# Kernel optimization log

Measured on AMD Instinct MI355X. Metric: run time of the kernel, lower is better.

Reference implementation:

```python
import jax, jax.numpy as jnp
import numpy as np

N_ATOMS = 100000
N_BONDS = 400000
ATOM_FDIM = 133
BOND_FDIM = 147
HIDDEN = 300
DEPTH = 3


def setup_inputs() -> dict:
    key = jax.random.key(0)
    ks = jax.random.split(key, 10)
    f_atoms = jax.random.normal(ks[0], (N_ATOMS, ATOM_FDIM), dtype=jnp.float32)
    f_bonds = jax.random.normal(ks[1], (N_BONDS, BOND_FDIM), dtype=jnp.float32)
    b2a = jax.random.randint(ks[2], (N_BONDS,), 0, N_ATOMS)
    b2revb = jax.random.randint(ks[3], (N_BONDS,), 0, N_BONDS)
    s_i = 1.0 / np.sqrt(BOND_FDIM)
    s_h = 1.0 / np.sqrt(HIDDEN)
    s_o = 1.0 / np.sqrt(ATOM_FDIM + HIDDEN)
    Wi_w = jax.random.uniform(ks[4], (HIDDEN, BOND_FDIM), jnp.float32, -s_i, s_i)
    Wi_b = jax.random.uniform(ks[5], (HIDDEN,), jnp.float32, -s_i, s_i)
    Wh_w = jax.random.uniform(ks[6], (HIDDEN, HIDDEN), jnp.float32, -s_h, s_h)
    Wh_b = jax.random.uniform(ks[7], (HIDDEN,), jnp.float32, -s_h, s_h)
    Wo_w = jax.random.uniform(ks[8], (HIDDEN, ATOM_FDIM + HIDDEN), jnp.float32, -s_o, s_o)
    Wo_b = jax.random.uniform(ks[9], (HIDDEN,), jnp.float32, -s_o, s_o)
    return {"f_atoms": f_atoms, "f_bonds": f_bonds, "b2a": b2a, "b2revb": b2revb,
            "Wi_w": Wi_w, "Wi_b": Wi_b, "Wh_w": Wh_w, "Wh_b": Wh_b,
            "Wo_w": Wo_w, "Wo_b": Wo_b}


def reference(f_atoms, f_bonds, b2a, b2revb, Wi_w, Wi_b, Wh_w, Wh_b, Wo_w, Wo_b):
    n_atoms = f_atoms.shape[0]
    # initial bond messages: [n_bonds, hidden]
    H_bonds = jax.nn.relu(f_bonds @ Wi_w.T + Wi_b)
    dest = b2a[b2revb]  # destination atom of each directed bond
    for _ in range(DEPTH - 1):
        # scatter-add bond messages onto destination atoms
        sum_msgs = jax.ops.segment_sum(H_bonds, dest, num_segments=n_atoms)
        # gather back to bonds from source atoms, subtract reverse-bond message
        msgs = sum_msgs[b2a] - H_bonds[b2revb]
        H_bonds = jax.nn.relu(H_bonds + msgs @ Wh_w.T + Wh_b)
    sum_msgs = jax.ops.segment_sum(H_bonds, dest, num_segments=n_atoms)
    H_atoms = jax.nn.relu(jnp.concatenate([f_atoms, sum_msgs], axis=1) @ Wo_w.T + Wo_b)
    return (H_atoms, H_bonds)
```

## Files before the change

kernel.cpp:

```cpp
#include <hip/hip_runtime.h>
#include <hip/hip_bf16.h>

#define NB 400000
#define NA 100000
#define AFD 133
#define BFD 147
#define HID 300
#define NP  320
#define SMP 304
#define NT  98

typedef short short8 __attribute__((ext_vector_type(8)));
typedef float f32x4 __attribute__((ext_vector_type(4)));

__device__ __forceinline__ ushort f2b(float f) {
    union { float f; unsigned u; } v; v.f = f;
    unsigned r = v.u + 0x7fffu + ((v.u >> 16) & 1u);
    return (ushort)(r >> 16);
}
__device__ __forceinline__ float b2f(ushort u) {
    union { unsigned u; float f; } v; v.u = ((unsigned)u) << 16;
    return v.f;
}

#define GLDS(gp, lp) __builtin_amdgcn_global_load_lds( \
    (const __attribute__((address_space(1))) void*)(gp), \
    (__attribute__((address_space(3))) void*)(lp), 16, 0, 0)


__global__ void pad_w_k(const float* __restrict__ W, ushort* __restrict__ Wp,
                        int N, int K, int Kp) {
    int idx = blockIdx.x * 256 + threadIdx.x;
    if (idx >= NP * Kp) return;
    int n = idx / Kp, k = idx - n * Kp;
    int t = k >> 5, kk = k & 31;
    int g = kk >> 3, s = kk & 7;
    int gp = g ^ ((n >> 1) & 3);
    ushort v = (n < N && k < K) ? f2b(W[n * K + k]) : (ushort)0;
    Wp[(size_t)t * 10240 + n * 32 + gp * 8 + s] = v;
}

__global__ void pad_bias_k(const float* __restrict__ bh, float* __restrict__ bhp) {
    int i = blockIdx.x * 256 + threadIdx.x;
    if (i < NP) bhp[i] = (i < HID) ? bh[i] : 0.f;
}

__global__ void dest_k(const int* __restrict__ b2a, const int* __restrict__ b2revb,
                       int* __restrict__ dest) {
    int b = blockIdx.x * 256 + threadIdx.x;
    if (b < NB) dest[b] = b2a[b2revb[b]];
}

__global__ void count_k(const int* __restrict__ dest, int* __restrict__ cnt) {
    int b = blockIdx.x * 256 + threadIdx.x;
    if (b < NB) atomicAdd(&cnt[dest[b]], 1);
}

__global__ void scanA_k(const int* __restrict__ cnt, int* __restrict__ tsum) {
    __shared__ int sm[256];
    const int tid = threadIdx.x;
    int base = blockIdx.x * 1024 + tid * 4;
    int s = 0;
#pragma unroll
    for (int j = 0; j < 4; ++j) { int i = base + j; if (i < NA) s += cnt[i]; }
    sm[tid] = s; __syncthreads();
    for (int o = 128; o > 0; o >>= 1) {
        if (tid < o) sm[tid] += sm[tid + o];
        __syncthreads();
    }
    if (tid == 0) tsum[blockIdx.x] = sm[0];
}

__global__ void scanB_k(const int* __restrict__ tsum, int* __restrict__ toff,
                        int* __restrict__ rs) {
    if (threadIdx.x == 0) {
        int run = 0;
        for (int t = 0; t < NT; ++t) { toff[t] = run; run += tsum[t]; }
        rs[NA] = run;
    }
}

__global__ void scanC_k(const int* __restrict__ cnt, const int* __restrict__ toff,
                        int* __restrict__ rs) {
    __shared__ int sm[256];
    const int tid = threadIdx.x;
    int base = blockIdx.x * 1024 + tid * 4;
    int v[4]; int s = 0;
#pragma unroll
    for (int j = 0; j < 4; ++j) {
        v[j] = (base + j < NA) ? cnt[base + j] : 0;
        s += v[j];
    }
    sm[tid] = s; __syncthreads();
    for (int o = 1; o < 256; o <<= 1) {
        int x = (tid >= o) ? sm[tid - o] : 0;
        __syncthreads();
        sm[tid] += x;
        __syncthreads();
    }
    int acc = sm[tid] - s + toff[blockIdx.x];
#pragma unroll
    for (int j = 0; j < 4; ++j) {
        if (base + j < NA) rs[base + j] = acc;
        acc += v[j];
    }
}

__global__ void scatter_k(const int* __restrict__ dest, const int* __restrict__ rs,
                          int* __restrict__ cur, int* __restrict__ bl) {
    int b = blockIdx.x * 256 + threadIdx.x;
    if (b >= NB) return;
    int a = dest[b];
    int pos = rs[a] + atomicAdd(&cur[a], 1);
    bl[pos] = b;
}

template<int MODE>
__global__ __launch_bounds__(512) void gemm_k(
    const float* __restrict__ F1, const float* __restrict__ Sum,
    const ushort* __restrict__ W, const float* __restrict__ bias,
    ushort* __restrict__ Cb, float* __restrict__ Cf, int M)
{
    constexpr int KP = (MODE == 0) ? 192 : 448;
    constexpr int TILES = KP / 32;
    static_assert(KP % 64 == 0 && TILES % 2 == 0, "XOR swizzle needs 128B rows, even tiles");
    __shared__ ushort As[128 * KP];
    __shared__ ushort Bs[2][320 * 32];

    const int tid = threadIdx.x;
    const int w = tid >> 6, lane = tid & 63;
    const int wr = w >> 2, wc = w & 3;
    const int g = lane >> 4, lr = lane & 15;
    const int m0 = blockIdx.x * 128;

    {
        const int row = tid >> 2, q = tid & 3;
        int grow = m0 + row;
        if (MODE == 2 && grow >= M) grow = M - 1;
        const int axw = (row & 7) << 4;
        char* abase = (char*)As + (size_t)row * (KP * 2);
#pragma unroll
        for (int t = 0; t < TILES; ++t) {
            const int k0 = t * 32 + q * 8;
            ushort o[8];
            if (MODE == 0) {
                const float* src = F1 + (size_t)grow * BFD;
#pragma unroll
                for (int s = 0; s < 8; ++s)
                    o[s] = (k0 + s < BFD) ? f2b(src[k0 + s]) : (ushort)0;
            } else {
#pragma unroll
                for (int s = 0; s < 8; ++s) {
                    int k = k0 + s;
                    float x = 0.f;
                    if (k < AFD) x = F1[(size_t)grow * AFD + k];
                    else if (k < AFD + SMP) x = Sum[(size_t)grow * SMP + (k - AFD)];
                    o[s] = f2b(x);
                }
            }
            ushort* dst = (ushort*)(abase + ((t * 64 + q * 16) ^ axw));
            *(ushort4*)dst       = make_ushort4(o[0], o[1], o[2], o[3]);
            *(ushort4*)(dst + 4) = make_ushort4(o[4], o[5], o[6], o[7]);
        }
    }

    auto stageB = [&](int t, int buf) {
        const ushort* wt = W + (size_t)t * 10240;
        ushort* bs = &Bs[buf][0];
        GLDS(wt + (size_t)w * 512 + lane * 8,        bs + w * 512);
        GLDS(wt + (size_t)(w + 8) * 512 + lane * 8,  bs + (w + 8) * 512);
        if (w < 4)
            GLDS(wt + (size_t)(w + 16) * 512 + lane * 8, bs + (w + 16) * 512);
    };

    f32x4 acc[4][5];
#pragma unroll
    for (int mi = 0; mi < 4; ++mi)
#pragma unroll
        for (int ni = 0; ni < 5; ++ni) acc[mi][ni] = (f32x4){0.f, 0.f, 0.f, 0.f};

    stageB(0, 0);
    __syncthreads();

    const int raxw = (lr & 7) << 4;
    const int bswz = (lr >> 1) & 3;
    for (int t = 0; t < TILES; ++t) {
        if (t + 1 < TILES) stageB(t + 1, (t + 1) & 1);
        const ushort* bs = &Bs[t & 1][0];
        short8 af[4];
#pragma unroll
        for (int mi = 0; mi < 4; ++mi) {
            const int r = wr * 64 + mi * 16 + lr;
            af[mi] = *(const short8*)((const char*)As + (size_t)r * (KP * 2)
                                      + ((t * 64 + g * 16) ^ raxw));
        }
#pragma unroll
        for (int ni = 0; ni < 5; ++ni) {
            const int c = wc * 80 + ni * 16 + lr;
            short8 bf = *(const short8*)&bs[c * 32 + ((g ^ bswz) << 3)];
#pragma unroll
            for (int mi = 0; mi < 4; ++mi)
                acc[mi][ni] = __builtin_amdgcn_mfma_f32_16x16x32_bf16(af[mi], bf, acc[mi][ni], 0, 0, 0);
        }
        __syncthreads();
    }

#pragma unroll
    for (int ni = 0; ni < 5; ++ni) {
        const int col = wc * 80 + ni * 16 + lr;
        const float bv = (col < HID) ? bias[col] : 0.f;
#pragma unroll
        for (int mi = 0; mi < 4; ++mi) {
            const int row0 = m0 + wr * 64 + mi * 16 + g * 4;
#pragma unroll
            for (int r = 0; r < 4; ++r) {
                const int row = row0 + r;
                float v = fmaxf(acc[mi][ni][r] + bv, 0.f);
                if (MODE == 2) {
                    if (col < HID && row < M) Cf[(size_t)row * HID + col] = v;
                } else {
                    Cb[(size_t)row * NP + col] = f2b(v);
                }
            }
        }
    }
}

__global__ __launch_bounds__(512) void gemm_a_k(
    const ushort* __restrict__ A, const ushort* __restrict__ W,
    ushort* __restrict__ C, int M)
{
    __shared__ ushort As[2][4][128][8];
    __shared__ ushort Bs[2][320 * 32];
    const int tid = threadIdx.x;
    const int w = tid >> 6, lane = tid & 63;
    const int wr = w >> 2, wc = w & 3;
    const int g = lane >> 4, lr = lane & 15;
    const int m0 = blockIdx.x * 128;

    const int q = w >> 1, r0 = (w & 1) * 64;
    int srow = m0 + r0 + lane; if (srow >= M) srow = M - 1;
    const ushort* aglob = A + (size_t)srow * NP + q * 8;

    f32x4 acc[4][5];
#pragma unroll
    for (int mi = 0; mi < 4; ++mi)
#pragma unroll
        for (int ni = 0; ni < 5; ++ni) acc[mi][ni] = (f32x4){0.f, 0.f, 0.f, 0.f};

    auto stageA = [&](int t, int buf) { GLDS(aglob + t * 32, &As[buf][q][r0][0]); };
    auto stageB = [&](int t, int buf) {
        const ushort* wt = W + (size_t)t * 10240;
        ushort* bs = &Bs[buf][0];
        GLDS(wt + (size_t)w * 512 + lane * 8,        bs + w * 512);
        GLDS(wt + (size_t)(w + 8) * 512 + lane * 8,  bs + (w + 8) * 512);
        if (w < 4)
            GLDS(wt + (size_t)(w + 16) * 512 + lane * 8, bs + (w + 16) * 512);
    };

    stageA(0, 0); stageB(0, 0);
    __syncthreads();

    const int bswz = (lr >> 1) & 3;
    for (int t = 0; t < 10; ++t) {
        if (t < 9) { stageA(t + 1, (t + 1) & 1); stageB(t + 1, (t + 1) & 1); }
        const int buf = t & 1;
        short8 af[4];
#pragma unroll
        for (int mi = 0; mi < 4; ++mi)
            af[mi] = *(const short8*)&As[buf][g][wr * 64 + mi * 16 + lr][0];
#pragma unroll
        for (int ni = 0; ni < 5; ++ni) {
            const int c = wc * 80 + ni * 16 + lr;
            short8 bf = *(const short8*)&Bs[buf][c * 32 + ((g ^ bswz) << 3)];
#pragma unroll
            for (int mi = 0; mi < 4; ++mi)
                acc[mi][ni] = __builtin_amdgcn_mfma_f32_16x16x32_bf16(af[mi], bf, acc[mi][ni], 0, 0, 0);
        }
        __syncthreads();
    }

#pragma unroll
    for (int ni = 0; ni < 5; ++ni) {
        const int col = wc * 80 + ni * 16 + lr;
#pragma unroll
        for (int mi = 0; mi < 4; ++mi) {
            const int row0 = m0 + wr * 64 + mi * 16 + g * 4;
#pragma unroll
            for (int r = 0; r < 4; ++r)
                if (row0 + r < M) C[(size_t)(row0 + r) * NP + col] = f2b(acc[mi][ni][r]);
        }
    }
}

template<bool OUTF>
__global__ __launch_bounds__(512) void gemm_u_k(
    const ushort* __restrict__ HbIn, const ushort* __restrict__ W,
    const ushort* __restrict__ SYa,
    const int* __restrict__ b2a, const int* __restrict__ b2revb,
    const float* __restrict__ bhp,
    ushort* __restrict__ HbOut, float* __restrict__ Hbonds)
{
    __shared__ ushort As[2][4][128][8];
    __shared__ ushort Bs[2][320 * 32];
    const int tid = threadIdx.x;
    const int w = tid >> 6, lane = tid & 63;
    const int wr = w >> 2, wc = w & 3;
    const int g = lane >> 4, lr = lane & 15;
    const int m0 = blockIdx.x * 128;

    const int q = w >> 1, r0 = (w & 1) * 64;
    const int rrow = b2revb[m0 + r0 + lane];
    const ushort* aglob = HbIn + (size_t)rrow * NP + q * 8;

    f32x4 acc[4][5];
#pragma unroll
    for (int mi = 0; mi < 4; ++mi)
#pragma unroll
        for (int ni = 0; ni < 5; ++ni) acc[mi][ni] = (f32x4){0.f, 0.f, 0.f, 0.f};

    auto stageA = [&](int t, int buf) { GLDS(aglob + t * 32, &As[buf][q][r0][0]); };
    auto stageB = [&](int t, int buf) {
        const ushort* wt = W + (size_t)t * 10240;
        ushort* bs = &Bs[buf][0];
        GLDS(wt + (size_t)w * 512 + lane * 8,        bs + w * 512);
        GLDS(wt + (size_t)(w + 8) * 512 + lane * 8,  bs + (w + 8) * 512);
        if (w < 4)
            GLDS(wt + (size_t)(w + 16) * 512 + lane * 8, bs + (w + 16) * 512);
    };

    stageA(0, 0); stageB(0, 0);
    __syncthreads();

    const int bswz = (lr >> 1) & 3;
    for (int t = 0; t < 10; ++t) {
        if (t < 9) { stageA(t + 1, (t + 1) & 1); stageB(t + 1, (t + 1) & 1); }
        const int buf = t & 1;
        short8 af[4];
#pragma unroll
        for (int mi = 0; mi < 4; ++mi)
            af[mi] = *(const short8*)&As[buf][g][wr * 64 + mi * 16 + lr][0];
#pragma unroll
        for (int ni = 0; ni < 5; ++ni) {
            const int c = wc * 80 + ni * 16 + lr;
            short8 bf = *(const short8*)&Bs[buf][c * 32 + ((g ^ bswz) << 3)];
#pragma unroll
            for (int mi = 0; mi < 4; ++mi)
                acc[mi][ni] = __builtin_amdgcn_mfma_f32_16x16x32_bf16(af[mi], bf, acc[mi][ni], 0, 0, 0);
        }
        __syncthreads();
    }

    float bv[5];
#pragma unroll
    for (int ni = 0; ni < 5; ++ni) bv[ni] = bhp[wc * 80 + ni * 16 + lr];
#pragma unroll
    for (int mi = 0; mi < 4; ++mi) {
#pragma unroll
        for (int r = 0; r < 4; ++r) {
            const int row = m0 + wr * 64 + mi * 16 + g * 4 + r;
            const int sa = b2a[row];
            const ushort* hp = &HbIn[(size_t)row * NP];
            const ushort* sp = &SYa[(size_t)sa * NP];
#pragma unroll
            for (int ni = 0; ni < 5; ++ni) {
                const int col = wc * 80 + ni * 16 + lr;
                float v = fmaxf(b2f(hp[col]) + b2f(sp[col]) - acc[mi][ni][r] + bv[ni], 0.f);
                HbOut[(size_t)row * NP + col] = f2b(v);
                if (OUTF && col < HID) Hbonds[(size_t)row * HID + col] = v;
            }
        }
    }
}

__global__ void seg_sum_bf16_k(const ushort* __restrict__ H, const int* __restrict__ rs,
                               const int* __restrict__ bl, ushort* __restrict__ SH) {
    int idx = blockIdx.x * 256 + threadIdx.x;
    if (idx >= NA * 40) return;
    int a = idx / 40, c = (idx - a * 40) * 8;
    int s0 = rs[a], s1 = rs[a + 1];
    float acc[8] = {0.f, 0.f, 0.f, 0.f, 0.f, 0.f, 0.f, 0.f};
    for (int j = s0; j < s1; ++j) {
        const ushort* p = &H[(size_t)bl[j] * NP + c];
        ushort4 u0 = *(const ushort4*)p, u1 = *(const ushort4*)(p + 4);
        acc[0] += b2f(u0.x); acc[1] += b2f(u0.y);
        acc[2] += b2f(u0.z); acc[3] += b2f(u0.w);
        acc[4] += b2f(u1.x); acc[5] += b2f(u1.y);
        acc[6] += b2f(u1.z); acc[7] += b2f(u1.w);
    }
    ushort* dst = &SH[(size_t)a * NP + c];
    *(ushort4*)dst       = make_ushort4(f2b(acc[0]), f2b(acc[1]), f2b(acc[2]), f2b(acc[3]));
    *(ushort4*)(dst + 4) = make_ushort4(f2b(acc[4]), f2b(acc[5]), f2b(acc[6]), f2b(acc[7]));
}

__global__ void seg_sum_csr_k(const ushort* __restrict__ Hb, const int* __restrict__ rs,
                              const int* __restrict__ bl, float* __restrict__ sum) {
    int idx = blockIdx.x * 256 + threadIdx.x;
    if (idx >= NA * 38) return;
    int a = idx / 38, c = (idx - a * 38) * 8;
    int s0 = rs[a], s1 = rs[a + 1];
    float acc[8] = {0.f, 0.f, 0.f, 0.f, 0.f, 0.f, 0.f, 0.f};
    for (int j = s0; j < s1; ++j) {
        const ushort* p = &Hb[(size_t)bl[j] * NP + c];
        ushort4 u0 = *(const ushort4*)p, u1 = *(const ushort4*)(p + 4);
        acc[0] += b2f(u0.x); acc[1] += b2f(u0.y);
        acc[2] += b2f(u0.z); acc[3] += b2f(u0.w);
        acc[4] += b2f(u1.x); acc[5] += b2f(u1.y);
        acc[6] += b2f(u1.z); acc[7] += b2f(u1.w);
    }
    float* dst = &sum[(size_t)a * SMP + c];
    *(float4*)dst       = make_float4(acc[0], acc[1], acc[2], acc[3]);
    *(float4*)(dst + 4) = make_float4(acc[4], acc[5], acc[6], acc[7]);
}

extern "C" void kernel_launch(void* const* d_in, const int* in_sizes, int n_in,
                              void* d_out, int out_size, void* d_ws, size_t ws_size,
                              hipStream_t stream) {
    const float* f_atoms = (const float*)d_in[0];
    const float* f_bonds = (const float*)d_in[1];
    const int*   b2a     = (const int*)d_in[2];
    const int*   b2revb  = (const int*)d_in[3];
    const float* Wi_w    = (const float*)d_in[4];
    const float* Wi_b    = (const float*)d_in[5];
    const float* Wh_w    = (const float*)d_in[6];
    const float* Wh_b    = (const float*)d_in[7];
    const float* Wo_w    = (const float*)d_in[8];
    const float* Wo_b    = (const float*)d_in[9];
    float* out = (float*)d_out;

    char* ws = (char*)d_ws;
    ushort* Hb0  = (ushort*)ws;            ws += (size_t)NB * NP * 2;
    ushort* Hb1  = (ushort*)ws;            ws += (size_t)NB * NP * 2;
    ushort* SHb  = (ushort*)ws;            ws += (size_t)NA * NP * 2;
    ushort* SYa  = (ushort*)ws;            ws += (size_t)NA * NP * 2;
    float*  sum  = (float*)ws;             ws += (size_t)NA * SMP * 4;
    int*    dest = (int*)ws;               ws += (size_t)NB * 4;
    ushort* Wp0  = (ushort*)ws;            ws += (size_t)6  * 10240 * 2;
    ushort* Wp1  = (ushort*)ws;            ws += (size_t)10 * 10240 * 2;
    ushort* Wp2  = (ushort*)ws;            ws += (size_t)14 * 10240 * 2;
    float*  bhp  = (float*)ws;             ws += (size_t)NP * 4;
    int*    cnt  = (int*)ws;               ws += (size_t)NA * 4;
    int*    cur  = (int*)ws;               ws += (size_t)NA * 4;
    int*    rs   = (int*)ws;               ws += (size_t)(NA + 1) * 4;
    int*    bl   = (int*)ws;               ws += (size_t)NB * 4;
    int*    tsum = (int*)ws;               ws += 128 * 4;
    int*    toff = (int*)ws;               ws += 128 * 4;
    float* Hatoms = out;
    float* Hbonds = out + (size_t)NA * HID;

    pad_w_k<<<(NP * 192 + 255) / 256, 256, 0, stream>>>(Wi_w, Wp0, HID, BFD, 192);
    pad_w_k<<<(NP * NP  + 255) / 256, 256, 0, stream>>>(Wh_w, Wp1, HID, HID, NP);
    pad_w_k<<<(NP * 448 + 255) / 256, 256, 0, stream>>>(Wo_w, Wp2, HID, AFD + HID, 448);
    pad_bias_k<<<2, 256, 0, stream>>>(Wh_b, bhp);
    dest_k<<<(NB + 255) / 256, 256, 0, stream>>>(b2a, b2revb, dest);
    hipMemsetAsync(cnt, 0, (size_t)NA * 4, stream);
    hipMemsetAsync(cur, 0, (size_t)NA * 4, stream);
    count_k<<<(NB + 255) / 256, 256, 0, stream>>>(dest, cnt);
    scanA_k<<<NT, 256, 0, stream>>>(cnt, tsum);
    scanB_k<<<1, 64, 0, stream>>>(tsum, toff, rs);
    scanC_k<<<NT, 256, 0, stream>>>(cnt, toff, rs);
    scatter_k<<<(NB + 255) / 256, 256, 0, stream>>>(dest, rs, cur, bl);

    gemm_k<0><<<NB / 128, 512, 0, stream>>>(
        f_bonds, nullptr, Wp0, Wi_b, Hb0, nullptr, NB);

    seg_sum_bf16_k<<<(NA * 40 + 255) / 256, 256, 0, stream>>>(Hb0, rs, bl, SHb);
    gemm_a_k<<<(NA + 127) / 128, 512, 0, stream>>>(SHb, Wp1, SYa, NA);
    gemm_u_k<false><<<NB / 128, 512, 0, stream>>>(
        Hb0, Wp1, SYa, b2a, b2revb, bhp, Hb1, nullptr);

    seg_sum_bf16_k<<<(NA * 40 + 255) / 256, 256, 0, stream>>>(Hb1, rs, bl, SHb);
    gemm_a_k<<<(NA + 127) / 128, 512, 0, stream>>>(SHb, Wp1, SYa, NA);
    gemm_u_k<true><<<NB / 128, 512, 0, stream>>>(
        Hb1, Wp1, SYa, b2a, b2revb, bhp, Hb0, Hbonds);

    seg_sum_csr_k<<<(NA * 38 + 255) / 256, 256, 0, stream>>>(Hb0, rs, bl, sum);
    gemm_k<2><<<(NA + 127) / 128, 512, 0, stream>>>(
        f_atoms, sum, Wp2, Wo_b, nullptr, Hatoms, NA);
}
```

Baseline: 1.680 ms.

## Stage GEMM epilogues through LDS for coalesced stores; reuse bf16 segment sum

The epilogues of the initial bond GEMM and the update GEMM now write accumulators into shared memory one column quarter at a time. Threads then read them back row-contiguous, so the global loads and stores for HbIn, SYa, HbOut and Hbonds are vectorized and coalesced instead of scattered 2-byte writes. The final segment sum reuses the bf16 kernel writing into SHb, and the output GEMM reads bf16 directly, removing the fp32 sum buffer and its conversion. The cost is four extra barrier phases per block plus an LDS round trip, and a slight precision loss because the final atom sums are now rounded to bf16.

```diff
diff --git a/kernel.cpp b/kernel.cpp
--- a/kernel.cpp
+++ b/kernel.cpp
@@ -7,7 +7,6 @@
 #define BFD 147
 #define HID 300
 #define NP  320
-#define SMP 304
 #define NT  98
 
 typedef short short8 __attribute__((ext_vector_type(8)));
@@ -117,15 +116,15 @@
 
 template<int MODE>
 __global__ __launch_bounds__(512) void gemm_k(
-    const float* __restrict__ F1, const float* __restrict__ Sum,
+    const float* __restrict__ F1, const ushort* __restrict__ SHb,
     const ushort* __restrict__ W, const float* __restrict__ bias,
     ushort* __restrict__ Cb, float* __restrict__ Cf, int M)
 {
     constexpr int KP = (MODE == 0) ? 192 : 448;
     constexpr int TILES = KP / 32;
     static_assert(KP % 64 == 0 && TILES % 2 == 0, "XOR swizzle needs 128B rows, even tiles");
-    __shared__ ushort As[128 * KP];
-    __shared__ ushort Bs[2][320 * 32];
+    __shared__ char smem[(128 * KP + 2 * 10240) * 2];
+    ushort (*Bs)[10240] = (ushort (*)[10240])(smem + 128 * KP * 2);
 
     const int tid = threadIdx.x;
     const int w = tid >> 6, lane = tid & 63;
@@ -138,7 +137,7 @@
         int grow = m0 + row;
         if (MODE == 2 && grow >= M) grow = M - 1;
         const int axw = (row & 7) << 4;
-        char* abase = (char*)As + (size_t)row * (KP * 2);
+        char* abase = smem + (size_t)row * (KP * 2);
 #pragma unroll
         for (int t = 0; t < TILES; ++t) {
             const int k0 = t * 32 + q * 8;
@@ -152,10 +151,8 @@
 #pragma unroll
                 for (int s = 0; s < 8; ++s) {
                     int k = k0 + s;
-                    float x = 0.f;
-                    if (k < AFD) x = F1[(size_t)grow * AFD + k];
-                    else if (k < AFD + SMP) x = Sum[(size_t)grow * SMP + (k - AFD)];
-                    o[s] = f2b(x);
+                    o[s] = (k < AFD) ? f2b(F1[(size_t)grow * AFD + k])
+                                     : SHb[(size_t)grow * NP + (k - AFD)];
                 }
             }
             ushort* dst = (ushort*)(abase + ((t * 64 + q * 16) ^ axw));
@@ -191,7 +188,7 @@
 #pragma unroll
         for (int mi = 0; mi < 4; ++mi) {
             const int r = wr * 64 + mi * 16 + lr;
-            af[mi] = *(const short8*)((const char*)As + (size_t)r * (KP * 2)
+            af[mi] = *(const short8*)(smem + (size_t)r * (KP * 2)
                                       + ((t * 64 + g * 16) ^ raxw));
         }
 #pragma unroll
@@ -205,21 +202,47 @@
         __syncthreads();
     }
 
-#pragma unroll
-    for (int ni = 0; ni < 5; ++ni) {
-        const int col = wc * 80 + ni * 16 + lr;
-        const float bv = (col < HID) ? bias[col] : 0.f;
-#pragma unroll
-        for (int mi = 0; mi < 4; ++mi) {
-            const int row0 = m0 + wr * 64 + mi * 16 + g * 4;
-#pragma unroll
-            for (int r = 0; r < 4; ++r) {
-                const int row = row0 + r;
-                float v = fmaxf(acc[mi][ni][r] + bv, 0.f);
-                if (MODE == 2) {
+    if (MODE == 0) {
+        float* EP = (float*)smem;
+        for (int ph = 0; ph < 4; ++ph) {
+            __syncthreads();
+            if (wc == ph) {
+#pragma unroll
+                for (int mi = 0; mi < 4; ++mi)
+#pragma unroll
+                    for (int ni = 0; ni < 5; ++ni) {
+                        const int ec = ni * 16 + lr;
+#pragma unroll
+                        for (int r = 0; r < 4; ++r)
+                            EP[(wr * 64 + mi * 16 + g * 4 + r) * 84 + ec] = acc[mi][ni][r];
+                    }
+            }
+            __syncthreads();
+            for (int it2 = tid; it2 < 2560; it2 += 512) {
+                const int row = it2 / 20, cc = (it2 - row * 20) * 4;
+                const int grow = m0 + row;
+                const int col = ph * 80 + cc;
+                float4 a = *(const float4*)&EP[row * 84 + cc];
+                float4 bb = (col < HID) ? *(const float4*)&bias[col]
+                                        : make_float4(0.f, 0.f, 0.f, 0.f);
+                *(ushort4*)&Cb[(size_t)grow * NP + col] =
+                    make_ushort4(f2b(fmaxf(a.x + bb.x, 0.f)), f2b(fmaxf(a.y + bb.y, 0.f)),
+                                 f2b(fmaxf(a.z + bb.z, 0.f)), f2b(fmaxf(a.w + bb.w, 0.f)));
+            }
+        }
+    } else {
+#pragma unroll
+        for (int ni = 0; ni < 5; ++ni) {
+            const int col = wc * 80 + ni * 16 + lr;
+            const float bv = (col < HID) ? bias[col] : 0.f;
+#pragma unroll
+            for (int mi = 0; mi < 4; ++mi) {
+                const int row0 = m0 + wr * 64 + mi * 16 + g * 4;
+#pragma unroll
+                for (int r = 0; r < 4; ++r) {
+                    const int row = row0 + r;
+                    float v = fmaxf(acc[mi][ni][r] + bv, 0.f);
                     if (col < HID && row < M) Cf[(size_t)row * HID + col] = v;
-                } else {
-                    Cb[(size_t)row * NP + col] = f2b(v);
                 }
             }
         }
@@ -231,7 +254,7 @@
     ushort* __restrict__ C, int M)
 {
     __shared__ ushort As[2][4][128][8];
-    __shared__ ushort Bs[2][320 * 32];
+    __shared__ ushort Bs[2][10240];
     const int tid = threadIdx.x;
     const int w = tid >> 6, lane = tid & 63;
     const int wr = w >> 2, wc = w & 3;
@@ -301,8 +324,9 @@
     const float* __restrict__ bhp,
     ushort* __restrict__ HbOut, float* __restrict__ Hbonds)
 {
-    __shared__ ushort As[2][4][128][8];
-    __shared__ ushort Bs[2][320 * 32];
+    __shared__ char smem[57344];
+    ushort (*As)[4][128][8] = (ushort (*)[4][128][8])smem;
+    ushort (*Bs)[10240] = (ushort (*)[10240])(smem + 16384);
     const int tid = threadIdx.x;
     const int w = tid >> 6, lane = tid & 63;
     const int wr = w >> 2, wc = w & 3;
@@ -351,24 +375,38 @@
         __syncthreads();
     }
 
-    float bv[5];
-#pragma unroll
-    for (int ni = 0; ni < 5; ++ni) bv[ni] = bhp[wc * 80 + ni * 16 + lr];
-#pragma unroll
-    for (int mi = 0; mi < 4; ++mi) {
-#pragma unroll
-        for (int r = 0; r < 4; ++r) {
-            const int row = m0 + wr * 64 + mi * 16 + g * 4 + r;
-            const int sa = b2a[row];
-            const ushort* hp = &HbIn[(size_t)row * NP];
-            const ushort* sp = &SYa[(size_t)sa * NP];
-#pragma unroll
-            for (int ni = 0; ni < 5; ++ni) {
-                const int col = wc * 80 + ni * 16 + lr;
-                float v = fmaxf(b2f(hp[col]) + b2f(sp[col]) - acc[mi][ni][r] + bv[ni], 0.f);
-                HbOut[(size_t)row * NP + col] = f2b(v);
-                if (OUTF && col < HID) Hbonds[(size_t)row * HID + col] = v;
-            }
+    float* EP = (float*)smem;
+    for (int ph = 0; ph < 4; ++ph) {
+        __syncthreads();
+        if (wc == ph) {
+#pragma unroll
+            for (int mi = 0; mi < 4; ++mi)
+#pragma unroll
+                for (int ni = 0; ni < 5; ++ni) {
+                    const int ec = ni * 16 + lr;
+#pragma unroll
+                    for (int r = 0; r < 4; ++r)
+                        EP[(wr * 64 + mi * 16 + g * 4 + r) * 84 + ec] = acc[mi][ni][r];
+                }
+        }
+        __syncthreads();
+        for (int it2 = tid; it2 < 2560; it2 += 512) {
+            const int row = it2 / 20, cc = (it2 - row * 20) * 4;
+            const int grow = m0 + row;
+            const int col = ph * 80 + cc;
+            float4 a = *(const float4*)&EP[row * 84 + cc];
+            const ushort4 h = *(const ushort4*)&HbIn[(size_t)grow * NP + col];
+            const ushort4 s = *(const ushort4*)&SYa[(size_t)b2a[grow] * NP + col];
+            const float4 bb = *(const float4*)&bhp[col];
+            float v0 = fmaxf(b2f(h.x) + b2f(s.x) - a.x + bb.x, 0.f);
+            float v1 = fmaxf(b2f(h.y) + b2f(s.y) - a.y + bb.y, 0.f);
+            float v2 = fmaxf(b2f(h.z) + b2f(s.z) - a.z + bb.z, 0.f);
+            float v3 = fmaxf(b2f(h.w) + b2f(s.w) - a.w + bb.w, 0.f);
+            *(ushort4*)&HbOut[(size_t)grow * NP + col] =
+                make_ushort4(f2b(v0), f2b(v1), f2b(v2), f2b(v3));
+            if (OUTF && col < HID)
+                *(float4*)&Hbonds[(size_t)grow * HID + col] =
+                    make_float4(v0, v1, v2, v3);
         }
     }
 }
@@ -393,26 +431,6 @@
     *(ushort4*)(dst + 4) = make_ushort4(f2b(acc[4]), f2b(acc[5]), f2b(acc[6]), f2b(acc[7]));
 }
 
-__global__ void seg_sum_csr_k(const ushort* __restrict__ Hb, const int* __restrict__ rs,
-                              const int* __restrict__ bl, float* __restrict__ sum) {
-    int idx = blockIdx.x * 256 + threadIdx.x;
-    if (idx >= NA * 38) return;
-    int a = idx / 38, c = (idx - a * 38) * 8;
-    int s0 = rs[a], s1 = rs[a + 1];
-    float acc[8] = {0.f, 0.f, 0.f, 0.f, 0.f, 0.f, 0.f, 0.f};
-    for (int j = s0; j < s1; ++j) {
-        const ushort* p = &Hb[(size_t)bl[j] * NP + c];
-        ushort4 u0 = *(const ushort4*)p, u1 = *(const ushort4*)(p + 4);
-        acc[0] += b2f(u0.x); acc[1] += b2f(u0.y);
-        acc[2] += b2f(u0.z); acc[3] += b2f(u0.w);
-        acc[4] += b2f(u1.x); acc[5] += b2f(u1.y);
-        acc[6] += b2f(u1.z); acc[7] += b2f(u1.w);
-    }
-    float* dst = &sum[(size_t)a * SMP + c];
-    *(float4*)dst       = make_float4(acc[0], acc[1], acc[2], acc[3]);
-    *(float4*)(dst + 4) = make_float4(acc[4], acc[5], acc[6], acc[7]);
-}
-
 extern "C" void kernel_launch(void* const* d_in, const int* in_sizes, int n_in,
                               void* d_out, int out_size, void* d_ws, size_t ws_size,
                               hipStream_t stream) {
@@ -433,7 +451,6 @@
     ushort* Hb1  = (ushort*)ws;            ws += (size_t)NB * NP * 2;
     ushort* SHb  = (ushort*)ws;            ws += (size_t)NA * NP * 2;
     ushort* SYa  = (ushort*)ws;            ws += (size_t)NA * NP * 2;
-    float*  sum  = (float*)ws;             ws += (size_t)NA * SMP * 4;
     int*    dest = (int*)ws;               ws += (size_t)NB * 4;
     ushort* Wp0  = (ushort*)ws;            ws += (size_t)6  * 10240 * 2;
     ushort* Wp1  = (ushort*)ws;            ws += (size_t)10 * 10240 * 2;
@@ -474,7 +491,7 @@
     gemm_u_k<true><<<NB / 128, 512, 0, stream>>>(
         Hb1, Wp1, SYa, b2a, b2revb, bhp, Hb0, Hbonds);
 
-    seg_sum_csr_k<<<(NA * 38 + 255) / 256, 256, 0, stream>>>(Hb0, rs, bl, sum);
+    seg_sum_bf16_k<<<(NA * 40 + 255) / 256, 256, 0, stream>>>(Hb0, rs, bl, SHb);
     gemm_k<2><<<(NA + 127) / 128, 512, 0, stream>>>(
-        f_atoms, sum, Wp2, Wo_b, nullptr, Hatoms, NA);
-}
+        f_atoms, SHb, Wp2, Wo_b, nullptr, Hatoms, NA);
+}
```

Measured after the change: 1.827 ms. +8.8%, slower.
